# Optimization experiments

Hardware: AMD Instinct MI355X
Metric: run time of the kernel (lower is better)

## Reference

```python
import jax, jax.numpy as jnp
import numpy as np

N_NODES = 50000
N_EDGES = 800000
IN_FEATS = 64
HID_FEATS = 64


def setup_inputs() -> dict:
    key = jax.random.key(0)
    ks = jax.random.split(key, 5)
    x = jax.random.normal(ks[0], (N_NODES, IN_FEATS), dtype=jnp.float32)
    src = jax.random.randint(ks[1], (N_EDGES,), 0, N_NODES)
    dst = jax.random.randint(ks[2], (N_EDGES,), 0, N_NODES)
    # GraphConv parameters (Glorot-ish init, bias zeros as in dgl defaults)
    W1 = jax.random.normal(ks[3], (IN_FEATS, HID_FEATS), dtype=jnp.float32) / np.sqrt(IN_FEATS)
    b1 = jnp.zeros((HID_FEATS,), dtype=jnp.float32)
    W2 = jax.random.normal(ks[4], (HID_FEATS, IN_FEATS), dtype=jnp.float32) / np.sqrt(HID_FEATS)
    b2 = jnp.zeros((IN_FEATS,), dtype=jnp.float32)
    return {"x": x, "src": src, "dst": dst, "W1": W1, "b1": b1, "W2": W2, "b2": b2}


def _graph_conv(x, src, dst, W, b, n_nodes):
    """dgl GraphConv with norm='both': D_dst^{-1/2} A D_src^{-1/2} X W + b."""
    ones = jnp.ones((src.shape[0],), dtype=x.dtype)
    deg_out = jax.ops.segment_sum(ones, src, num_segments=n_nodes)
    deg_in = jax.ops.segment_sum(ones, dst, num_segments=n_nodes)
    norm_out = jnp.where(deg_out > 0, jax.lax.rsqrt(jnp.maximum(deg_out, 1.0)), 0.0)
    norm_in = jnp.where(deg_in > 0, jax.lax.rsqrt(jnp.maximum(deg_in, 1.0)), 0.0)
    h = x * norm_out[:, None]                                  # [N, F] scaled by src norm
    agg = jax.ops.segment_sum(h[src], dst, num_segments=n_nodes)  # gather over edges + scatter-add
    return (agg * norm_in[:, None]) @ W + b


def reference(x, src, dst, W1, b1, W2, b2):
    n, d = x.shape
    # dHdx: conv -> tanh -> conv
    y = jnp.tanh(_graph_conv(x, src, dst, W1, b1, n))
    y = _graph_conv(y, src, dst, W2, b2, n)
    # J = cat([I[d//2:], -I[:d//2]])  -> symplectic [[0, I], [-I, 0]]
    I = jnp.eye(d, dtype=x.dtype)
    J = jnp.concatenate([I[d // 2:], -I[: d // 2]], axis=0)
    # get_D is undefined in the source module; treated as zero dissipation term.
    return y @ J.T
```

## Files before the change

### kernel.cpp

```cpp
#include <hip/hip_runtime.h>
#include <hip/hip_bf16.h>
#include <math.h>

#define N_NODES 50000
#define N_EDGES 800000
#define F 64
#define NPAD 50048
#define NBLK ((N_NODES + 255) / 256)

#define P_HIST 256
#define CHUNK (N_EDGES / P_HIST)
#define WORDS8 12500
#define RBLK8 ((WORDS8 + 255) / 256)
#define RSPLIT 4
#define WR (WORDS8 / RSPLIT)
#define HBLK (P_HIST * RSPLIT)

#define TW 20
#define RV3BLK (WORDS8 / TW)
#define TS 260

#define LROW 36
#define LBLK ((N_NODES + 31) / 32)

typedef short short8 __attribute__((ext_vector_type(8)));
typedef float f32x4 __attribute__((ext_vector_type(4)));

__device__ inline unsigned short f2bf(float f) {
    unsigned u = __float_as_uint(f);
    unsigned r = (u + 0x7fffu + ((u >> 16) & 1u)) >> 16;
    return (unsigned short)r;
}
__device__ inline float bf2f(unsigned v) { return __uint_as_float(v << 16); }
__device__ inline float bf2f_hi(unsigned v) { return __uint_as_float(v & 0xffff0000u); }

__device__ inline unsigned wave_incl_scan(unsigned v, int lane) {
    #pragma unroll
    for (int d = 1; d < 64; d <<= 1) {
        unsigned u = __shfl_up(v, d, 64);
        if (lane >= d) v += u;
    }
    return v;
}


__global__ __launch_bounds__(256) void hist2_kernel(
    const int* __restrict__ src, const int* __restrict__ dst,
    unsigned* __restrict__ histd, unsigned* __restrict__ hists)
{
    __shared__ unsigned ldd[WR];
    __shared__ unsigned lsd[WR];
    int bid = blockIdx.x, t = threadIdx.x;
    int p = bid >> 2, r = bid & 3;
    int e0 = p * CHUNK;
    unsigned wbase = (unsigned)(r * WR);
    for (int i = t; i < WR; i += 256) { ldd[i] = 0; lsd[i] = 0; }
    __syncthreads();
    for (int i = t; i < CHUNK; i += 256) {
        int d = dst[e0 + i];
        int s = src[e0 + i];
        unsigned wd = ((unsigned)d >> 2) - wbase;
        unsigned ws = ((unsigned)s >> 2) - wbase;
        if (wd < WR) atomicAdd(&ldd[wd], 1u << ((d & 3) * 8));
        if (ws < WR) atomicAdd(&lsd[ws], 1u << ((s & 3) * 8));
    }
    __syncthreads();
    unsigned* outd = histd + (size_t)p * WORDS8 + r * WR;
    unsigned* outs = hists + (size_t)p * WORDS8 + r * WR;
    for (int i = t; i < WR; i += 256) { outd[i] = ldd[i]; outs[i] = lsd[i]; }
}

__global__ __launch_bounds__(256) void reduce_v3_kernel(
    unsigned* __restrict__ histd, const unsigned* __restrict__ hists,
    float* __restrict__ norm_in, float* __restrict__ norm_out,
    int* __restrict__ row_off, unsigned* __restrict__ wordsum,
    const float* __restrict__ x, unsigned* __restrict__ xb)
{
    __shared__ unsigned lds[TW * TS];
    __shared__ float normv[TW * 4];
    int t = threadIdx.x, b = blockIdx.x;
    int lane = t & 63, ww = t >> 6;
    int w0 = b * TW;

    {
        uint4* gp = (uint4*)(histd + (size_t)t * WORDS8 + w0);
        #pragma unroll
        for (int i = 0; i < TW / 4; ++i) {
            uint4 v = gp[i];
            lds[(i * 4 + 0) * TS + t] = v.x;
            lds[(i * 4 + 1) * TS + t] = v.y;
            lds[(i * 4 + 2) * TS + t] = v.z;
            lds[(i * 4 + 3) * TS + t] = v.w;
        }
    }
    __syncthreads();
    #pragma unroll
    for (int k = 0; k < TW / 4; ++k) {
        int lw = ww + k * 4;
        uint4 h = *(uint4*)(lds + lw * TS + 4 * lane);
        unsigned lsum = h.x + h.y + h.z + h.w;
        unsigned inc = lsum;
        #pragma unroll
        for (int d = 1; d < 64; d <<= 1) {
            unsigned u = __shfl_up(inc, d, 64);
            if (lane >= d) inc += u;
        }
        unsigned run = inc - lsum;
        uint4 o;
        o.x = run; run += h.x;
        o.y = run; run += h.y;
        o.z = run; run += h.z;
        o.w = run;
        *(uint4*)(lds + lw * TS + 4 * lane) = o;
        unsigned total = __shfl(inc, 63, 64);
        if (lane == 0) {
            int w = w0 + lw;
            unsigned d0 = total & 255u, d1 = (total >> 8) & 255u;
            unsigned d2 = (total >> 16) & 255u, d3 = total >> 24;
            norm_in[4 * w]     = d0 ? rsqrtf((float)d0) : 0.f;
            norm_in[4 * w + 1] = d1 ? rsqrtf((float)d1) : 0.f;
            norm_in[4 * w + 2] = d2 ? rsqrtf((float)d2) : 0.f;
            norm_in[4 * w + 3] = d3 ? rsqrtf((float)d3) : 0.f;
            int4 r;
            r.x = 0; r.y = (int)d0; r.z = (int)(d0 + d1); r.w = (int)(d0 + d1 + d2);
            *(int4*)(row_off + 4 * w) = r;
            wordsum[w] = d0 + d1 + d2 + d3;
        }
    }
    __syncthreads();
    {
        uint4* gp = (uint4*)(histd + (size_t)t * WORDS8 + w0);
        #pragma unroll
        for (int i = 0; i < TW / 4; ++i) {
            uint4 v;
            v.x = lds[(i * 4 + 0) * TS + t];
            v.y = lds[(i * 4 + 1) * TS + t];
            v.z = lds[(i * 4 + 2) * TS + t];
            v.w = lds[(i * 4 + 3) * TS + t];
            gp[i] = v;
        }
    }
    __syncthreads();

    {
        const uint4* gp = (const uint4*)(hists + (size_t)t * WORDS8 + w0);
        #pragma unroll
        for (int i = 0; i < TW / 4; ++i) {
            uint4 v = gp[i];
            lds[(i * 4 + 0) * TS + t] = v.x;
            lds[(i * 4 + 1) * TS + t] = v.y;
            lds[(i * 4 + 2) * TS + t] = v.z;
            lds[(i * 4 + 3) * TS + t] = v.w;
        }
    }
    __syncthreads();
    #pragma unroll
    for (int k = 0; k < TW / 4; ++k) {
        int lw = ww + k * 4;
        uint4 h = *(uint4*)(lds + lw * TS + 4 * lane);
        unsigned s = h.x + h.y + h.z + h.w;
        #pragma unroll
        for (int d = 1; d < 64; d <<= 1) s += __shfl_xor(s, d, 64);
        if (lane == 0) {
            int w = w0 + lw;
            unsigned t0 = s & 255u, t1 = (s >> 8) & 255u;
            unsigned t2 = (s >> 16) & 255u, t3 = s >> 24;
            float n0 = t0 ? rsqrtf((float)t0) : 0.f;
            float n1 = t1 ? rsqrtf((float)t1) : 0.f;
            float n2 = t2 ? rsqrtf((float)t2) : 0.f;
            float n3 = t3 ? rsqrtf((float)t3) : 0.f;
            norm_out[4 * w]     = n0;
            norm_out[4 * w + 1] = n1;
            norm_out[4 * w + 2] = n2;
            norm_out[4 * w + 3] = n3;
            normv[4 * lw]     = n0;
            normv[4 * lw + 1] = n1;
            normv[4 * lw + 2] = n2;
            normv[4 * lw + 3] = n3;
        }
    }
    __syncthreads();

    {
        int nb0 = w0 * 4;
        const float2* xp = (const float2*)x;
        for (int i = t; i < TW * 4 * 32; i += 256) {
            int ln = i >> 5;
            int c  = i & 31;
            float wv = normv[ln];
            float2 v = xp[(size_t)(nb0 + ln) * 32 + c];
            xb[(size_t)(nb0 + ln) * 32 + c] =
                (unsigned)f2bf(v.x * wv) | ((unsigned)f2bf(v.y * wv) << 16);
        }
    }
}

__global__ __launch_bounds__(256) void scanw_kernel(
    const unsigned* __restrict__ wordsum, int* __restrict__ row_off,
    unsigned* __restrict__ blockSums)
{
    __shared__ unsigned wsum[4];
    int t = threadIdx.x, b = blockIdx.x;
    int w = b * 256 + t;
    unsigned v = (w < WORDS8) ? wordsum[w] : 0u;
    int lane = t & 63, wid = t >> 6;
    unsigned inc = wave_incl_scan(v, lane);
    if (lane == 63) wsum[wid] = inc;
    __syncthreads();
    if (t == 0) {
        unsigned acc = 0;
        #pragma unroll
        for (int q = 0; q < 4; ++q) { unsigned x2 = wsum[q]; wsum[q] = acc; acc += x2; }
    }
    __syncthreads();
    unsigned excl = inc - v + wsum[wid];
    if (w < WORDS8) {
        int4 r = *(int4*)(row_off + 4 * w);
        r.x += (int)excl; r.y += (int)excl; r.z += (int)excl; r.w += (int)excl;
        *(int4*)(row_off + 4 * w) = r;
    }
    if (t == 255) blockSums[b] = excl + v;
}

__global__ __launch_bounds__(256) void scan_fin_kernel(
    const unsigned* __restrict__ blockSums, int* __restrict__ row_off)
{
    __shared__ unsigned off_s;
    int t = threadIdx.x, b = blockIdx.x;
    if (t < 64) {
        unsigned v = (t < b) ? blockSums[t] : 0u;
        #pragma unroll
        for (int d = 1; d < 64; d <<= 1) v += __shfl_xor(v, d, 64);
        if (t == 0) off_s = v;
    }
    __syncthreads();
    int off = (int)off_s;
    int w = b * 256 + t;
    if (w < WORDS8) {
        int4 r = *(int4*)(row_off + 4 * w);
        r.x += off; r.y += off; r.z += off; r.w += off;
        *(int4*)(row_off + 4 * w) = r;
    }
    if (w == 0) row_off[N_NODES] = N_EDGES;
}

__global__ __launch_bounds__(256) void scatter2_kernel(
    const int* __restrict__ src, const int* __restrict__ dst,
    const int* __restrict__ row_off, const unsigned* __restrict__ histd,
    int* __restrict__ csr_src)
{
    __shared__ unsigned rk[WR];
    __shared__ unsigned pf[WR];
    int bid = blockIdx.x, t = threadIdx.x;
    int p = bid >> 2, r = bid & 3;
    int e0 = p * CHUNK;
    unsigned wbase = (unsigned)(r * WR);
    const unsigned* pref = histd + (size_t)p * WORDS8 + r * WR;
    for (int i = t; i < WR; i += 256) { rk[i] = 0; pf[i] = pref[i]; }
    __syncthreads();
    for (int i = t; i < CHUNK; i += 256) {
        int d = dst[e0 + i];
        int s = src[e0 + i];
        unsigned wd = ((unsigned)d >> 2) - wbase;
        if (wd < WR) {
            int sh = (d & 3) * 8;
            unsigned old = atomicAdd(&rk[wd], 1u << sh);
            unsigned rank = (old >> sh) & 255u;
            unsigned pre  = (pf[wd] >> sh) & 255u;
            csr_src[row_off[d] + (int)(pre + rank)] = s;
        }
    }
}


__global__ __launch_bounds__(256) void degrees_kernel(
    const int* __restrict__ src, const int* __restrict__ dst,
    unsigned* __restrict__ deg_out_u, unsigned* __restrict__ deg_in_u)
{
    int e = blockIdx.x * 256 + threadIdx.x;
    if (e < N_EDGES) {
        atomicAdd(&deg_out_u[src[e]], 1u);
        atomicAdd(&deg_in_u[dst[e]], 1u);
    }
}

__global__ __launch_bounds__(256) void fb_scan_a_kernel(
    const unsigned* __restrict__ deg_in_u, const unsigned* __restrict__ deg_out_u,
    float* __restrict__ norm_out, float* __restrict__ norm_in,
    int* __restrict__ row_off, unsigned* __restrict__ blockSums)
{
    __shared__ unsigned wsum[4];
    int t = threadIdx.x, b = blockIdx.x;
    int idx = b * 256 + t;
    unsigned v = 0, dout = 0;
    if (idx < N_NODES) { v = deg_in_u[idx]; dout = deg_out_u[idx]; }
    int lane = t & 63, wid = t >> 6;
    unsigned inc = wave_incl_scan(v, lane);
    if (lane == 63) wsum[wid] = inc;
    __syncthreads();
    if (t == 0) {
        unsigned acc = 0;
        #pragma unroll
        for (int q = 0; q < 4; ++q) { unsigned x2 = wsum[q]; wsum[q] = acc; acc += x2; }
    }
    __syncthreads();
    unsigned excl = inc - v + wsum[wid];
    if (idx < N_NODES) {
        row_off[idx] = (int)excl;
        norm_in[idx]  = v    ? rsqrtf((float)v)    : 0.f;
        norm_out[idx] = dout ? rsqrtf((float)dout) : 0.f;
    }
    if (t == 255) blockSums[b] = excl + v;
}

__global__ __launch_bounds__(256) void fb_scan_b_kernel(
    const unsigned* __restrict__ blockSums, unsigned* __restrict__ blockOff, int cnt)
{
    __shared__ unsigned wsum[4];
    int t = threadIdx.x;
    unsigned v = (t < cnt) ? blockSums[t] : 0u;
    int lane = t & 63, wid = t >> 6;
    unsigned inc = wave_incl_scan(v, lane);
    if (lane == 63) wsum[wid] = inc;
    __syncthreads();
    if (t == 0) {
        unsigned acc = 0;
        #pragma unroll
        for (int q = 0; q < 4; ++q) { unsigned x2 = wsum[q]; wsum[q] = acc; acc += x2; }
    }
    __syncthreads();
    if (t < cnt) blockOff[t] = inc - v + wsum[wid];
}

__global__ __launch_bounds__(256) void fb_scan_c_kernel(
    const unsigned* __restrict__ blockOff, int* __restrict__ row_off,
    unsigned* __restrict__ cursor)
{
    int idx = blockIdx.x * 256 + threadIdx.x;
    if (idx < N_NODES) {
        int v = row_off[idx] + (int)blockOff[blockIdx.x];
        row_off[idx] = v;
        cursor[idx] = (unsigned)v;
    }
    if (idx == 0) row_off[N_NODES] = N_EDGES;
}

__global__ __launch_bounds__(256) void fb_csr_fill_kernel(
    const int* __restrict__ src, const int* __restrict__ dst,
    unsigned* __restrict__ cursor, int* __restrict__ csr_src)
{
    int e = blockIdx.x * 256 + threadIdx.x;
    if (e < N_EDGES) {
        unsigned p = atomicAdd(&cursor[dst[e]], 1u);
        csr_src[p] = src[e];
    }
}


__global__ __launch_bounds__(256) void prescale_kernel(
    const float* __restrict__ x, const float* __restrict__ norm_out,
    unsigned* __restrict__ xb)
{
    int t = blockIdx.x * 256 + threadIdx.x;
    if (t < N_NODES * 32) {
        int n = t >> 5;
        float w = norm_out[n];
        float2 v = ((const float2*)x)[t];
        xb[t] = (unsigned)f2bf(v.x * w) | ((unsigned)f2bf(v.y * w) << 16);
    }
}

__device__ inline void block_agg32(
    const unsigned* __restrict__ tab, const float* __restrict__ norm_in,
    const int* __restrict__ row_off, const int* __restrict__ csr_src,
    int nb, unsigned* lds)
{
    int tid = threadIdx.x;
    int wid = tid >> 6, lane = tid & 63;
    int g = lane >> 3, lp = lane & 7;
    int m = wid * 8 + g;
    int n = nb + m;
    float a0 = 0.f, a1 = 0.f, a2 = 0.f, a3 = 0.f;
    float a4 = 0.f, a5 = 0.f, a6 = 0.f, a7 = 0.f;
    float w = 0.f;
    if (n < N_NODES) {
        int beg = row_off[n];
        int end = row_off[n + 1];
        w = norm_in[n];
        int e = beg;
        for (; e + 3 < end; e += 4) {
            int s0 = csr_src[e], s1 = csr_src[e + 1];
            int s2 = csr_src[e + 2], s3 = csr_src[e + 3];
            uint4 v0 = *(const uint4*)(tab + (size_t)s0 * 32 + lp * 4);
            uint4 v1 = *(const uint4*)(tab + (size_t)s1 * 32 + lp * 4);
            uint4 v2 = *(const uint4*)(tab + (size_t)s2 * 32 + lp * 4);
            uint4 v3 = *(const uint4*)(tab + (size_t)s3 * 32 + lp * 4);
            a0 += bf2f(v0.x & 0xffffu); a1 += bf2f_hi(v0.x);
            a2 += bf2f(v0.y & 0xffffu); a3 += bf2f_hi(v0.y);
            a4 += bf2f(v0.z & 0xffffu); a5 += bf2f_hi(v0.z);
            a6 += bf2f(v0.w & 0xffffu); a7 += bf2f_hi(v0.w);
            a0 += bf2f(v1.x & 0xffffu); a1 += bf2f_hi(v1.x);
            a2 += bf2f(v1.y & 0xffffu); a3 += bf2f_hi(v1.y);
            a4 += bf2f(v1.z & 0xffffu); a5 += bf2f_hi(v1.z);
            a6 += bf2f(v1.w & 0xffffu); a7 += bf2f_hi(v1.w);
            a0 += bf2f(v2.x & 0xffffu); a1 += bf2f_hi(v2.x);
            a2 += bf2f(v2.y & 0xffffu); a3 += bf2f_hi(v2.y);
            a4 += bf2f(v2.z & 0xffffu); a5 += bf2f_hi(v2.z);
            a6 += bf2f(v2.w & 0xffffu); a7 += bf2f_hi(v2.w);
            a0 += bf2f(v3.x & 0xffffu); a1 += bf2f_hi(v3.x);
            a2 += bf2f(v3.y & 0xffffu); a3 += bf2f_hi(v3.y);
            a4 += bf2f(v3.z & 0xffffu); a5 += bf2f_hi(v3.z);
            a6 += bf2f(v3.w & 0xffffu); a7 += bf2f_hi(v3.w);
        }
        for (; e < end; ++e) {
            int s0 = csr_src[e];
            uint4 v0 = *(const uint4*)(tab + (size_t)s0 * 32 + lp * 4);
            a0 += bf2f(v0.x & 0xffffu); a1 += bf2f_hi(v0.x);
            a2 += bf2f(v0.y & 0xffffu); a3 += bf2f_hi(v0.y);
            a4 += bf2f(v0.z & 0xffffu); a5 += bf2f_hi(v0.z);
            a6 += bf2f(v0.w & 0xffffu); a7 += bf2f_hi(v0.w);
        }
    }
    uint4 o;
    o.x = (unsigned)f2bf(a0 * w) | ((unsigned)f2bf(a1 * w) << 16);
    o.y = (unsigned)f2bf(a2 * w) | ((unsigned)f2bf(a3 * w) << 16);
    o.z = (unsigned)f2bf(a4 * w) | ((unsigned)f2bf(a5 * w) << 16);
    o.w = (unsigned)f2bf(a6 * w) | ((unsigned)f2bf(a7 * w) << 16);
    *(uint4*)(lds + m * LROW + lp * 4) = o;
}

__global__ __launch_bounds__(256) void layer1_fused_kernel(
    const unsigned* __restrict__ tab, const float* __restrict__ norm_in,
    const float* __restrict__ norm_out, const int* __restrict__ row_off,
    const int* __restrict__ csr_src, const float* __restrict__ Wm,
    const float* __restrict__ bias, unsigned short* __restrict__ hb)
{
    __shared__ unsigned lds[32 * LROW];
    int tid = threadIdx.x;
    int wid = tid >> 6, lane = tid & 63;
    int q = lane >> 4, lp16 = lane & 15;
    int nb = blockIdx.x * 32;

    short8 bfrag[2];
    #pragma unroll
    for (int kt = 0; kt < 2; ++kt)
        #pragma unroll
        for (int j = 0; j < 8; ++j)
            bfrag[kt][j] = (short)f2bf(Wm[(kt * 32 + q * 8 + j) * F + wid * 16 + lp16]);

    block_agg32(tab, norm_in, row_off, csr_src, nb, lds);
    __syncthreads();

    int nn = wid * 16 + lp16;
    float bv = bias[nn];
    #pragma unroll
    for (int rg = 0; rg < 2; ++rg) {
        short8 afrag[2];
        #pragma unroll
        for (int kt = 0; kt < 2; ++kt)
            afrag[kt] = *(const short8*)(lds + (rg * 16 + lp16) * LROW + kt * 16 + q * 4);
        f32x4 acc = (f32x4){0.f, 0.f, 0.f, 0.f};
        #pragma unroll
        for (int kt = 0; kt < 2; ++kt)
            acc = __builtin_amdgcn_mfma_f32_16x16x32_bf16(afrag[kt], bfrag[kt], acc, 0, 0, 0);
        #pragma unroll
        for (int r = 0; r < 4; ++r) {
            int row = nb + rg * 16 + q * 4 + r;
            if (row < N_NODES) {
                float z = tanhf(acc[r] + bv) * norm_out[row];
                hb[(size_t)row * F + nn] = f2bf(z);
            }
        }
    }
}

__global__ __launch_bounds__(256) void layer2_fused_kernel(
    const unsigned* __restrict__ tab, const float* __restrict__ norm_in,
    const int* __restrict__ row_off, const int* __restrict__ csr_src,
    const float* __restrict__ Wm, const float* __restrict__ bias,
    float* __restrict__ out)
{
    __shared__ unsigned lds[32 * LROW];
    int tid = threadIdx.x;
    int wid = tid >> 6, lane = tid & 63;
    int q = lane >> 4, lp16 = lane & 15;
    int nb = blockIdx.x * 32;

    short8 bfrag[2];
    #pragma unroll
    for (int kt = 0; kt < 2; ++kt)
        #pragma unroll
        for (int j = 0; j < 8; ++j)
            bfrag[kt][j] = (short)f2bf(Wm[(kt * 32 + q * 8 + j) * F + wid * 16 + lp16]);

    block_agg32(tab, norm_in, row_off, csr_src, nb, lds);
    __syncthreads();

    int nn = wid * 16 + lp16;
    float bv = bias[nn];
    int oc = (nn + 32) & 63;
    float sgn = (nn < 32) ? -1.f : 1.f;
    #pragma unroll
    for (int rg = 0; rg < 2; ++rg) {
        short8 afrag[2];
        #pragma unroll
        for (int kt = 0; kt < 2; ++kt)
            afrag[kt] = *(const short8*)(lds + (rg * 16 + lp16) * LROW + kt * 16 + q * 4);
        f32x4 acc = (f32x4){0.f, 0.f, 0.f, 0.f};
        #pragma unroll
        for (int kt = 0; kt < 2; ++kt)
            acc = __builtin_amdgcn_mfma_f32_16x16x32_bf16(afrag[kt], bfrag[kt], acc, 0, 0, 0);
        #pragma unroll
        for (int r = 0; r < 4; ++r) {
            int row = nb + rg * 16 + q * 4 + r;
            if (row < N_NODES) {
                float z = acc[r] + bv;
                out[(size_t)row * F + oc] = sgn * z;
            }
        }
    }
}

extern "C" void kernel_launch(void* const* d_in, const int* in_sizes, int n_in,
                              void* d_out, int out_size, void* d_ws, size_t ws_size,
                              hipStream_t stream) {
    const float* x   = (const float*)d_in[0];
    const int*   src = (const int*)d_in[1];
    const int*   dst = (const int*)d_in[2];
    const float* W1  = (const float*)d_in[3];
    const float* b1  = (const float*)d_in[4];
    const float* W2  = (const float*)d_in[5];
    const float* b2  = (const float*)d_in[6];
    float* out = (float*)d_out;

    unsigned* ws = (unsigned*)d_ws;
    float*    norm_out = (float*)ws;
    float*    norm_in  = (float*)(ws + NPAD);
    int*      row_off  = (int*)(ws + 2 * NPAD);
    int*      csr_src  = (int*)(ws + 3 * NPAD);
    unsigned* xb       = ws + 3 * NPAD + N_EDGES;
    unsigned* hbu      = xb + (size_t)NPAD * 32;
    unsigned* blockSums= hbu + (size_t)NPAD * 32;
    unsigned* blockOff = blockSums + 256;
    unsigned* wordsum  = blockOff + 256;
    unsigned* tail     = wordsum + WORDS8;
    unsigned* histd = tail;
    unsigned* hists = histd + (size_t)P_HIST * WORDS8;
    size_t need_new = ((size_t)(tail - ws) + 2 * (size_t)P_HIST * WORDS8) * 4;

    if (ws_size >= need_new) {
        hist2_kernel<<<HBLK, 256, 0, stream>>>(src, dst, histd, hists);
        reduce_v3_kernel<<<RV3BLK, 256, 0, stream>>>(histd, hists, norm_in, norm_out, row_off, wordsum, x, xb);
        scanw_kernel<<<RBLK8, 256, 0, stream>>>(wordsum, row_off, blockSums);
        scan_fin_kernel<<<RBLK8, 256, 0, stream>>>(blockSums, row_off);
        scatter2_kernel<<<HBLK, 256, 0, stream>>>(src, dst, row_off, histd, csr_src);
    } else {
        unsigned* deg_out_u = tail;
        unsigned* deg_in_u  = tail + NPAD;
        unsigned* cursor    = tail + 2 * NPAD;
        hipMemsetAsync(deg_out_u, 0, 2 * NPAD * sizeof(unsigned), stream);
        degrees_kernel<<<(N_EDGES + 255) / 256, 256, 0, stream>>>(src, dst, deg_out_u, deg_in_u);
        fb_scan_a_kernel<<<NBLK, 256, 0, stream>>>(deg_in_u, deg_out_u, norm_out, norm_in, row_off, blockSums);
        fb_scan_b_kernel<<<1, 256, 0, stream>>>(blockSums, blockOff, NBLK);
        fb_scan_c_kernel<<<NBLK, 256, 0, stream>>>(blockOff, row_off, cursor);
        fb_csr_fill_kernel<<<(N_EDGES + 255) / 256, 256, 0, stream>>>(src, dst, cursor, csr_src);
        prescale_kernel<<<(N_NODES * 32 + 255) / 256, 256, 0, stream>>>(x, norm_out, xb);
    }

    layer1_fused_kernel<<<LBLK, 256, 0, stream>>>(
        xb, norm_in, norm_out, row_off, csr_src, W1, b1, (unsigned short*)hbu);

    layer2_fused_kernel<<<LBLK, 256, 0, stream>>>(
        hbu, norm_in, row_off, csr_src, W2, b2, out);
}
```

Measured before the change: 163.0 us.

## Halve histogram partitions, widen hist/scatter blocks, merge two-pass scan into one

Cuts the number of edge partitions for the per-partition histograms from 256 to 128 and runs the hist and scatter kernels with 512 threads per block. The reduce kernel is reshaped so each column of 128 partitions is loaded by two half-blocks and scanned with two entries per lane. The block-sum scan and fix-up kernels are replaced by one kernel in which each block re-reduces all preceding word sums itself. This removes a launch and halves the histogram traffic, at the cost of fewer, larger blocks and redundant prefix reads in the scan.

After: 162.3 us (median of 2 runs). No clear change (-0.4%).

```diff
diff --git a/kernel.cpp b/kernel.cpp
--- a/kernel.cpp
+++ b/kernel.cpp
@@ -8,7 +8,7 @@
 #define NPAD 50048
 #define NBLK ((N_NODES + 255) / 256)
 
-#define P_HIST 256
+#define P_HIST 128
 #define CHUNK (N_EDGES / P_HIST)
 #define WORDS8 12500
 #define RBLK8 ((WORDS8 + 255) / 256)
@@ -18,7 +18,7 @@
 
 #define TW 20
 #define RV3BLK (WORDS8 / TW)
-#define TS 260
+#define TS 132
 
 #define LROW 36
 #define LBLK ((N_NODES + 31) / 32)
@@ -44,7 +44,7 @@
 }
 
 
-__global__ __launch_bounds__(256) void hist2_kernel(
+__global__ __launch_bounds__(512) void hist2_kernel(
     const int* __restrict__ src, const int* __restrict__ dst,
     unsigned* __restrict__ histd, unsigned* __restrict__ hists)
 {
@@ -54,9 +54,9 @@
     int p = bid >> 2, r = bid & 3;
     int e0 = p * CHUNK;
     unsigned wbase = (unsigned)(r * WR);
-    for (int i = t; i < WR; i += 256) { ldd[i] = 0; lsd[i] = 0; }
-    __syncthreads();
-    for (int i = t; i < CHUNK; i += 256) {
+    for (int i = t; i < WR; i += 512) { ldd[i] = 0; lsd[i] = 0; }
+    __syncthreads();
+    for (int i = t; i < CHUNK; i += 512) {
         int d = dst[e0 + i];
         int s = src[e0 + i];
         unsigned wd = ((unsigned)d >> 2) - wbase;
@@ -67,7 +67,7 @@
     __syncthreads();
     unsigned* outd = histd + (size_t)p * WORDS8 + r * WR;
     unsigned* outs = hists + (size_t)p * WORDS8 + r * WR;
-    for (int i = t; i < WR; i += 256) { outd[i] = ldd[i]; outs[i] = lsd[i]; }
+    for (int i = t; i < WR; i += 512) { outd[i] = ldd[i]; outs[i] = lsd[i]; }
 }
 
 __global__ __launch_bounds__(256) void reduce_v3_kernel(
@@ -81,24 +81,30 @@
     int t = threadIdx.x, b = blockIdx.x;
     int lane = t & 63, ww = t >> 6;
     int w0 = b * TW;
+    int c = t & 127, hf = t >> 7;
 
     {
-        uint4* gp = (uint4*)(histd + (size_t)t * WORDS8 + w0);
-        #pragma unroll
-        for (int i = 0; i < TW / 4; ++i) {
-            uint4 v = gp[i];
-            lds[(i * 4 + 0) * TS + t] = v.x;
-            lds[(i * 4 + 1) * TS + t] = v.y;
-            lds[(i * 4 + 2) * TS + t] = v.z;
-            lds[(i * 4 + 3) * TS + t] = v.w;
+        const unsigned* gp = histd + (size_t)c * WORDS8 + w0;
+        if (hf == 0) {
+            uint4 a = *(const uint4*)(gp);
+            uint4 b4 = *(const uint4*)(gp + 4);
+            uint4 c4 = *(const uint4*)(gp + 8);
+            lds[0*TS+c]=a.x;  lds[1*TS+c]=a.y;  lds[2*TS+c]=a.z;  lds[3*TS+c]=a.w;
+            lds[4*TS+c]=b4.x; lds[5*TS+c]=b4.y; lds[6*TS+c]=b4.z; lds[7*TS+c]=b4.w;
+            lds[8*TS+c]=c4.x; lds[9*TS+c]=c4.y; lds[10*TS+c]=c4.z; lds[11*TS+c]=c4.w;
+        } else {
+            uint4 a = *(const uint4*)(gp + 12);
+            uint4 b4 = *(const uint4*)(gp + 16);
+            lds[12*TS+c]=a.x;  lds[13*TS+c]=a.y;  lds[14*TS+c]=a.z;  lds[15*TS+c]=a.w;
+            lds[16*TS+c]=b4.x; lds[17*TS+c]=b4.y; lds[18*TS+c]=b4.z; lds[19*TS+c]=b4.w;
         }
     }
     __syncthreads();
     #pragma unroll
     for (int k = 0; k < TW / 4; ++k) {
         int lw = ww + k * 4;
-        uint4 h = *(uint4*)(lds + lw * TS + 4 * lane);
-        unsigned lsum = h.x + h.y + h.z + h.w;
+        uint2 h = *(uint2*)(lds + lw * TS + 2 * lane);
+        unsigned lsum = h.x + h.y;
         unsigned inc = lsum;
         #pragma unroll
         for (int d = 1; d < 64; d <<= 1) {
@@ -106,12 +112,10 @@
             if (lane >= d) inc += u;
         }
         unsigned run = inc - lsum;
-        uint4 o;
+        uint2 o;
         o.x = run; run += h.x;
-        o.y = run; run += h.y;
-        o.z = run; run += h.z;
-        o.w = run;
-        *(uint4*)(lds + lw * TS + 4 * lane) = o;
+        o.y = run;
+        *(uint2*)(lds + lw * TS + 2 * lane) = o;
         unsigned total = __shfl(inc, 63, 64);
         if (lane == 0) {
             int w = w0 + lw;
@@ -129,36 +133,44 @@
     }
     __syncthreads();
     {
-        uint4* gp = (uint4*)(histd + (size_t)t * WORDS8 + w0);
-        #pragma unroll
-        for (int i = 0; i < TW / 4; ++i) {
-            uint4 v;
-            v.x = lds[(i * 4 + 0) * TS + t];
-            v.y = lds[(i * 4 + 1) * TS + t];
-            v.z = lds[(i * 4 + 2) * TS + t];
-            v.w = lds[(i * 4 + 3) * TS + t];
-            gp[i] = v;
+        unsigned* gp = histd + (size_t)c * WORDS8 + w0;
+        if (hf == 0) {
+            uint4 a, b4, c4;
+            a.x=lds[0*TS+c];  a.y=lds[1*TS+c];  a.z=lds[2*TS+c];  a.w=lds[3*TS+c];
+            b4.x=lds[4*TS+c]; b4.y=lds[5*TS+c]; b4.z=lds[6*TS+c]; b4.w=lds[7*TS+c];
+            c4.x=lds[8*TS+c]; c4.y=lds[9*TS+c]; c4.z=lds[10*TS+c]; c4.w=lds[11*TS+c];
+            *(uint4*)(gp) = a; *(uint4*)(gp + 4) = b4; *(uint4*)(gp + 8) = c4;
+        } else {
+            uint4 a, b4;
+            a.x=lds[12*TS+c];  a.y=lds[13*TS+c];  a.z=lds[14*TS+c];  a.w=lds[15*TS+c];
+            b4.x=lds[16*TS+c]; b4.y=lds[17*TS+c]; b4.z=lds[18*TS+c]; b4.w=lds[19*TS+c];
+            *(uint4*)(gp + 12) = a; *(uint4*)(gp + 16) = b4;
         }
     }
     __syncthreads();
 
     {
-        const uint4* gp = (const uint4*)(hists + (size_t)t * WORDS8 + w0);
-        #pragma unroll
-        for (int i = 0; i < TW / 4; ++i) {
-            uint4 v = gp[i];
-            lds[(i * 4 + 0) * TS + t] = v.x;
-            lds[(i * 4 + 1) * TS + t] = v.y;
-            lds[(i * 4 + 2) * TS + t] = v.z;
-            lds[(i * 4 + 3) * TS + t] = v.w;
+        const unsigned* gp = hists + (size_t)c * WORDS8 + w0;
+        if (hf == 0) {
+            uint4 a = *(const uint4*)(gp);
+            uint4 b4 = *(const uint4*)(gp + 4);
+            uint4 c4 = *(const uint4*)(gp + 8);
+            lds[0*TS+c]=a.x;  lds[1*TS+c]=a.y;  lds[2*TS+c]=a.z;  lds[3*TS+c]=a.w;
+            lds[4*TS+c]=b4.x; lds[5*TS+c]=b4.y; lds[6*TS+c]=b4.z; lds[7*TS+c]=b4.w;
+            lds[8*TS+c]=c4.x; lds[9*TS+c]=c4.y; lds[10*TS+c]=c4.z; lds[11*TS+c]=c4.w;
+        } else {
+            uint4 a = *(const uint4*)(gp + 12);
+            uint4 b4 = *(const uint4*)(gp + 16);
+            lds[12*TS+c]=a.x;  lds[13*TS+c]=a.y;  lds[14*TS+c]=a.z;  lds[15*TS+c]=a.w;
+            lds[16*TS+c]=b4.x; lds[17*TS+c]=b4.y; lds[18*TS+c]=b4.z; lds[19*TS+c]=b4.w;
         }
     }
     __syncthreads();
     #pragma unroll
     for (int k = 0; k < TW / 4; ++k) {
         int lw = ww + k * 4;
-        uint4 h = *(uint4*)(lds + lw * TS + 4 * lane);
-        unsigned s = h.x + h.y + h.z + h.w;
+        uint2 h = *(uint2*)(lds + lw * TS + 2 * lane);
+        unsigned s = h.x + h.y;
         #pragma unroll
         for (int d = 1; d < 64; d <<= 1) s += __shfl_xor(s, d, 64);
         if (lane == 0) {
@@ -186,65 +198,50 @@
         const float2* xp = (const float2*)x;
         for (int i = t; i < TW * 4 * 32; i += 256) {
             int ln = i >> 5;
-            int c  = i & 31;
+            int col = i & 31;
             float wv = normv[ln];
-            float2 v = xp[(size_t)(nb0 + ln) * 32 + c];
-            xb[(size_t)(nb0 + ln) * 32 + c] =
+            float2 v = xp[(size_t)(nb0 + ln) * 32 + col];
+            xb[(size_t)(nb0 + ln) * 32 + col] =
                 (unsigned)f2bf(v.x * wv) | ((unsigned)f2bf(v.y * wv) << 16);
         }
     }
 }
 
-__global__ __launch_bounds__(256) void scanw_kernel(
-    const unsigned* __restrict__ wordsum, int* __restrict__ row_off,
-    unsigned* __restrict__ blockSums)
+__global__ __launch_bounds__(256) void scan_all_kernel(
+    const unsigned* __restrict__ wordsum, int* __restrict__ row_off)
 {
     __shared__ unsigned wsum[4];
+    __shared__ unsigned redsum[4];
     int t = threadIdx.x, b = blockIdx.x;
-    int w = b * 256 + t;
+    int base = b * 256;
+    int lane = t & 63, wid = t >> 6;
+    unsigned acc = 0;
+    for (int i = t; i < base; i += 256) acc += wordsum[i];
+    #pragma unroll
+    for (int d = 1; d < 64; d <<= 1) acc += __shfl_xor(acc, d, 64);
+    if (lane == 0) redsum[wid] = acc;
+    int w = base + t;
     unsigned v = (w < WORDS8) ? wordsum[w] : 0u;
-    int lane = t & 63, wid = t >> 6;
     unsigned inc = wave_incl_scan(v, lane);
     if (lane == 63) wsum[wid] = inc;
     __syncthreads();
     if (t == 0) {
-        unsigned acc = 0;
-        #pragma unroll
-        for (int q = 0; q < 4; ++q) { unsigned x2 = wsum[q]; wsum[q] = acc; acc += x2; }
-    }
-    __syncthreads();
-    unsigned excl = inc - v + wsum[wid];
+        unsigned a = 0;
+        #pragma unroll
+        for (int q = 0; q < 4; ++q) { unsigned x2 = wsum[q]; wsum[q] = a; a += x2; }
+    }
+    __syncthreads();
+    unsigned prior = redsum[0] + redsum[1] + redsum[2] + redsum[3];
+    unsigned excl = inc - v + wsum[wid] + prior;
     if (w < WORDS8) {
         int4 r = *(int4*)(row_off + 4 * w);
         r.x += (int)excl; r.y += (int)excl; r.z += (int)excl; r.w += (int)excl;
         *(int4*)(row_off + 4 * w) = r;
     }
-    if (t == 255) blockSums[b] = excl + v;
-}
-
-__global__ __launch_bounds__(256) void scan_fin_kernel(
-    const unsigned* __restrict__ blockSums, int* __restrict__ row_off)
-{
-    __shared__ unsigned off_s;
-    int t = threadIdx.x, b = blockIdx.x;
-    if (t < 64) {
-        unsigned v = (t < b) ? blockSums[t] : 0u;
-        #pragma unroll
-        for (int d = 1; d < 64; d <<= 1) v += __shfl_xor(v, d, 64);
-        if (t == 0) off_s = v;
-    }
-    __syncthreads();
-    int off = (int)off_s;
-    int w = b * 256 + t;
-    if (w < WORDS8) {
-        int4 r = *(int4*)(row_off + 4 * w);
-        r.x += off; r.y += off; r.z += off; r.w += off;
-        *(int4*)(row_off + 4 * w) = r;
-    }
     if (w == 0) row_off[N_NODES] = N_EDGES;
 }
 
-__global__ __launch_bounds__(256) void scatter2_kernel(
+__global__ __launch_bounds__(512) void scatter2_kernel(
     const int* __restrict__ src, const int* __restrict__ dst,
     const int* __restrict__ row_off, const unsigned* __restrict__ histd,
     int* __restrict__ csr_src)
@@ -256,9 +253,9 @@
     int e0 = p * CHUNK;
     unsigned wbase = (unsigned)(r * WR);
     const unsigned* pref = histd + (size_t)p * WORDS8 + r * WR;
-    for (int i = t; i < WR; i += 256) { rk[i] = 0; pf[i] = pref[i]; }
-    __syncthreads();
-    for (int i = t; i < CHUNK; i += 256) {
+    for (int i = t; i < WR; i += 512) { rk[i] = 0; pf[i] = pref[i]; }
+    __syncthreads();
+    for (int i = t; i < CHUNK; i += 512) {
         int d = dst[e0 + i];
         int s = src[e0 + i];
         unsigned wd = ((unsigned)d >> 2) - wbase;
@@ -549,11 +546,10 @@
     size_t need_new = ((size_t)(tail - ws) + 2 * (size_t)P_HIST * WORDS8) * 4;
 
     if (ws_size >= need_new) {
-        hist2_kernel<<<HBLK, 256, 0, stream>>>(src, dst, histd, hists);
+        hist2_kernel<<<HBLK, 512, 0, stream>>>(src, dst, histd, hists);
         reduce_v3_kernel<<<RV3BLK, 256, 0, stream>>>(histd, hists, norm_in, norm_out, row_off, wordsum, x, xb);
-        scanw_kernel<<<RBLK8, 256, 0, stream>>>(wordsum, row_off, blockSums);
-        scan_fin_kernel<<<RBLK8, 256, 0, stream>>>(blockSums, row_off);
-        scatter2_kernel<<<HBLK, 256, 0, stream>>>(src, dst, row_off, histd, csr_src);
+        scan_all_kernel<<<RBLK8, 256, 0, stream>>>(wordsum, row_off);
+        scatter2_kernel<<<HBLK, 512, 0, stream>>>(src, dst, row_off, histd, csr_src);
     } else {
         unsigned* deg_out_u = tail;
         unsigned* deg_in_u  = tail + NPAD;
```
